# Kernel optimization log

Hardware: AMD Instinct MI355X
Metric: run time of the kernel (lower is better)

## Reference

```python
import jax, jax.numpy as jnp
import numpy as np

N, E, U, EF, STEPS = 5000, 40000, 64, 16, 4


def setup_inputs() -> dict:
    key = jax.random.key(0)
    ks = jax.random.split(key, 7)
    node_features = jax.random.normal(ks[0], (N, U), dtype=jnp.float32)
    edge_features = jax.random.normal(ks[1], (E, EF), dtype=jnp.float32)
    pair_indices = jax.random.randint(ks[2], (E, 2), 0, N, dtype=jnp.int32)
    # EdgeNetwork params: kernel (efc, nfc*nfc), bias (nfc*nfc,)
    edge_kernel = jax.random.normal(ks[3], (EF, U * U), dtype=jnp.float32) * 0.05
    edge_bias = jnp.zeros((U * U,), dtype=jnp.float32)
    # Keras GRUCell (reset_after=True): kernel (in, 3u), recurrent (u, 3u), bias (2, 3u)
    gru_kernel = jax.random.normal(ks[4], (U, 3 * U), dtype=jnp.float32) * 0.05
    gru_recurrent_kernel = jax.random.normal(ks[5], (U, 3 * U), dtype=jnp.float32) * 0.05
    gru_bias = jnp.zeros((2, 3 * U), dtype=jnp.float32)
    return {
        "node_features": node_features,
        "edge_features": edge_features,
        "pair_indices": pair_indices,
        "edge_kernel": edge_kernel,
        "edge_bias": edge_bias,
        "gru_kernel": gru_kernel,
        "gru_recurrent_kernel": gru_recurrent_kernel,
        "gru_bias": gru_bias,
    }


def _gru_cell(x, h, kernel, rkernel, bias):
    # Keras GRUCell math with reset_after=True
    u = h.shape[-1]
    mx = x @ kernel + bias[0]          # [N, 3u]
    mh = h @ rkernel + bias[1]         # [N, 3u]
    xz, xr, xh = mx[:, :u], mx[:, u:2 * u], mx[:, 2 * u:]
    iz, ir, ih = mh[:, :u], mh[:, u:2 * u], mh[:, 2 * u:]
    z = jax.nn.sigmoid(xz + iz)
    r = jax.nn.sigmoid(xr + ir)
    hh = jnp.tanh(xh + r * ih)
    return z * h + (1.0 - z) * hh


def reference(node_features, edge_features, pair_indices, edge_kernel, edge_bias,
              gru_kernel, gru_recurrent_kernel, gru_bias):
    n = node_features.shape[0]
    u = node_features.shape[1]  # units (pad_length = 0 since nfc == units)
    src = pair_indices[:, 0]
    nbr = pair_indices[:, 1]
    # Edge matrices are loop-invariant: [E, u, u]
    edge_mats = (edge_features @ edge_kernel + edge_bias).reshape(-1, u, u)
    h = node_features
    for _ in range(STEPS):
        nb = h[nbr]                                    # gather [E, u]
        msg = jnp.einsum('eij,ej->ei', edge_mats, nb)  # per-edge matvec
        agg = jax.ops.segment_sum(msg, src, num_segments=n)  # scatter-sum [N, u]
        h = _gru_cell(agg, h, gru_kernel, gru_recurrent_kernel, gru_bias)
    return h
```

## Files before the change

kernel.cpp:

```cpp
#include <hip/hip_runtime.h>
#include <math.h>

#define NN 5000
#define NE 40000
#define UU 64
#define FE 16
#define FEP 17
#define KD (FEP*UU)
#define LDK (KD+8)
#define NSTEPS 4
#define NT 8
#define NB (NN/NT)
#define EMAX 256
#define CH 8

typedef _Float16 half8 __attribute__((ext_vector_type(8)));
typedef float f32x4 __attribute__((ext_vector_type(4)));

__device__ __forceinline__ float sigm(float x){ return 1.f/(1.f + __expf(-x)); }
__device__ __forceinline__ int rfl(int x){ return __builtin_amdgcn_readfirstlane(x); }

#define WBN (UU*KD)
#define GTN (192*64)
__global__ void build_k(const float* __restrict__ ek, const float* __restrict__ eb,
                        const float* __restrict__ gk, const float* __restrict__ rk,
                        _Float16* __restrict__ wb, _Float16* __restrict__ gkt,
                        _Float16* __restrict__ rkt, int* __restrict__ offs){
  int tid = blockIdx.x*blockDim.x + threadIdx.x;
  if (tid <= NN) offs[tid] = 0;
  if (tid < WBN){
    int i = tid / KD, k = tid - i*KD;
    int f = k >> 6, j = k & 63;
    float v = (f < FE) ? ek[f*4096 + i*64 + j] : eb[i*64 + j];
    wb[tid] = (_Float16)v;
  } else if (tid < WBN + GTN){
    int r = tid - WBN; int n = r >> 6, k = r & 63;
    gkt[r] = (_Float16)gk[k*192 + n];
  } else if (tid < WBN + 2*GTN){
    int r = tid - WBN - GTN; int n = r >> 6, k = r & 63;
    rkt[r] = (_Float16)rk[k*192 + n];
  }
}

__global__ void hist_k(const int* __restrict__ pair, int* __restrict__ hist){
  int e = blockIdx.x*blockDim.x + threadIdx.x;
  if (e < NE) atomicAdd(&hist[pair[2*e]], 1);
}

__global__ void scan_k(int* __restrict__ offs, int* __restrict__ cursor){
  __shared__ int s[1024];
  const int PER = 5;
  int t = threadIdx.x;
  int base = t*PER;
  int loc[PER]; int sum = 0;
  #pragma unroll
  for (int q=0;q<PER;++q){ int idx = base+q; int v = (idx<NN)?offs[idx]:0; loc[q]=v; sum+=v; }
  s[t] = sum; __syncthreads();
  for (int off=1; off<1024; off<<=1){
    int v = (t>=off) ? s[t-off] : 0;
    __syncthreads();
    s[t] += v;
    __syncthreads();
  }
  int run = s[t] - sum;
  #pragma unroll
  for (int q=0;q<PER;++q){ int idx = base+q;
    if (idx<NN){ offs[idx]=run; cursor[idx]=run; run+=loc[q]; } }
  if (t==1023) offs[NN] = run;
}

__global__ void scatter_k(const int* __restrict__ pair, int* __restrict__ cursor,
                          int* __restrict__ eid){
  int e = blockIdx.x*blockDim.x + threadIdx.x;
  if (e < NE){ int pos = atomicAdd(&cursor[pair[2*e]], 1); eid[pos] = e; }
}

__global__ void sortsub_k(const int* __restrict__ offs, int* __restrict__ eid){
  int v = blockIdx.x*blockDim.x + threadIdx.x;
  if (v >= NN) return;
  int b = offs[v], e = offs[v+1];
  for (int i=b+1; i<e; ++i){
    int key = eid[i]; int j = i-1;
    while (j>=b && eid[j]>key){ eid[j+1]=eid[j]; --j; }
    eid[j+1] = key;
  }
}

__global__ __launch_bounds__(512) void step_k(const float* __restrict__ h_in,
        float* __restrict__ h_out,
        const int* __restrict__ pair, const float* __restrict__ ef,
        const int* __restrict__ offs, const int* __restrict__ eid,
        const _Float16* __restrict__ wb, const _Float16* __restrict__ gkt,
        const _Float16* __restrict__ rkt, const float* __restrict__ gb){
  __shared__ _Float16 Gs[NT*LDK];
  __shared__ int      enbr[EMAX];
  __shared__ int      eedg[EMAX];
  __shared__ _Float16 aggT[NT*72];
  __shared__ _Float16 hT[NT*72];

  int tid = threadIdx.x;
  int w = tid >> 6, lane = tid & 63;
  int r16 = lane & 15, kh = lane >> 4;
  int vb = blockIdx.x * NT;

  int ebase = offs[vb];
  int ecnt  = offs[vb + NT] - ebase;

  for (int i=tid; i<ecnt; i+=512){
    int e = eid[ebase + i];
    enbr[i] = pair[2*e + 1];
    eedg[i] = e;
  }
  hT[w*72 + lane] = (_Float16)h_in[(size_t)(vb + w)*64 + lane];
  __syncthreads();

  {
    int myb = offs[vb + w]     - ebase;
    int mye = offs[vb + w + 1] - ebase;
    float g[FEP];
    #pragma unroll
    for (int f=0;f<FEP;++f) g[f] = 0.f;
    for (int c0=myb; c0<mye; c0+=CH){
      float hj[CH];
      #pragma unroll
      for (int q=0;q<CH;++q){ int i=c0+q;
        if (i<mye){ int nb = rfl(enbr[i]); hj[q] = h_in[(size_t)nb*64 + lane]; }
        else hj[q] = 0.f; }
      #pragma unroll
      for (int q=0;q<CH;++q){ int i=c0+q;
        if (i<mye){
          int e = rfl(eedg[i]);
          const float4* er = (const float4*)(ef + (size_t)e*FE);
          float4 e0 = er[0], e1 = er[1], e2 = er[2], e3 = er[3];
          g[ 0]=fmaf(e0.x,hj[q],g[ 0]); g[ 1]=fmaf(e0.y,hj[q],g[ 1]);
          g[ 2]=fmaf(e0.z,hj[q],g[ 2]); g[ 3]=fmaf(e0.w,hj[q],g[ 3]);
          g[ 4]=fmaf(e1.x,hj[q],g[ 4]); g[ 5]=fmaf(e1.y,hj[q],g[ 5]);
          g[ 6]=fmaf(e1.z,hj[q],g[ 6]); g[ 7]=fmaf(e1.w,hj[q],g[ 7]);
          g[ 8]=fmaf(e2.x,hj[q],g[ 8]); g[ 9]=fmaf(e2.y,hj[q],g[ 9]);
          g[10]=fmaf(e2.z,hj[q],g[10]); g[11]=fmaf(e2.w,hj[q],g[11]);
          g[12]=fmaf(e3.x,hj[q],g[12]); g[13]=fmaf(e3.y,hj[q],g[13]);
          g[14]=fmaf(e3.z,hj[q],g[14]); g[15]=fmaf(e3.w,hj[q],g[15]);
          g[16] += hj[q];
        } }
    }
    #pragma unroll
    for (int f=0;f<FEP;++f) Gs[w*LDK + f*64 + lane] = (_Float16)g[f];
  }
  __syncthreads();

  if (w < 4){
    f32x4 acc = {0.f,0.f,0.f,0.f};
    const _Float16* ap = Gs + (r16 & 7)*LDK + kh*8;
    const _Float16* bp = wb + (size_t)(w*16 + r16)*KD + kh*8;
    #pragma unroll 2
    for (int k0=0; k0<KD; k0+=32){
      half8 a = *(const half8*)(ap + k0);
      half8 b = *(const half8*)(bp + k0);
      acc = __builtin_amdgcn_mfma_f32_16x16x32_f16(a, b, acc, 0, 0, 0);
    }
    if (kh < 2){
      #pragma unroll
      for (int r=0;r<4;++r) aggT[(kh*4+r)*72 + w*16 + r16] = (_Float16)acc[r];
    }
  }
  __syncthreads();

  if (w < 4){
    int uw = w*16 + r16;
    const _Float16* az = aggT + (r16 & 7)*72 + kh*8;
    const _Float16* ah = hT   + (r16 & 7)*72 + kh*8;
    f32x4 mxz={0.f,0.f,0.f,0.f}, mxr=mxz, mxh=mxz, mhz=mxz, mhr=mxz, mhh=mxz;
    #pragma unroll
    for (int ks=0; ks<2; ++ks){
      half8 aa = *(const half8*)(az + ks*32);
      half8 hh = *(const half8*)(ah + ks*32);
      half8 bz = *(const half8*)(gkt + (size_t)(      uw)*64 + ks*32 + kh*8);
      half8 br = *(const half8*)(gkt + (size_t)( 64 + uw)*64 + ks*32 + kh*8);
      half8 bh = *(const half8*)(gkt + (size_t)(128 + uw)*64 + ks*32 + kh*8);
      half8 cz = *(const half8*)(rkt + (size_t)(      uw)*64 + ks*32 + kh*8);
      half8 cr = *(const half8*)(rkt + (size_t)( 64 + uw)*64 + ks*32 + kh*8);
      half8 ch = *(const half8*)(rkt + (size_t)(128 + uw)*64 + ks*32 + kh*8);
      mxz = __builtin_amdgcn_mfma_f32_16x16x32_f16(aa, bz, mxz, 0,0,0);
      mxr = __builtin_amdgcn_mfma_f32_16x16x32_f16(aa, br, mxr, 0,0,0);
      mxh = __builtin_amdgcn_mfma_f32_16x16x32_f16(aa, bh, mxh, 0,0,0);
      mhz = __builtin_amdgcn_mfma_f32_16x16x32_f16(hh, cz, mhz, 0,0,0);
      mhr = __builtin_amdgcn_mfma_f32_16x16x32_f16(hh, cr, mhr, 0,0,0);
      mhh = __builtin_amdgcn_mfma_f32_16x16x32_f16(hh, ch, mhh, 0,0,0);
    }
    if (kh < 2){
      float b0z = gb[uw],      b0r = gb[64+uw],  b0h = gb[128+uw];
      float b1z = gb[192+uw],  b1r = gb[256+uw], b1h = gb[320+uw];
      #pragma unroll
      for (int r=0;r<4;++r){
        int row = vb + kh*4 + r;
        float z  = sigm(mxz[r] + b0z + mhz[r] + b1z);
        float rr = sigm(mxr[r] + b0r + mhr[r] + b1r);
        float hc = tanhf(mxh[r] + b0h + rr*(mhh[r] + b1h));
        float hold = h_in[(size_t)row*64 + uw];
        h_out[(size_t)row*64 + uw] = z*hold + (1.f - z)*hc;
      }
    }
  }
}

extern "C" void kernel_launch(void* const* d_in, const int* in_sizes, int n_in,
                              void* d_out, int out_size, void* d_ws, size_t ws_size,
                              hipStream_t stream){
  const float* nodef = (const float*)d_in[0];
  const float* edgef = (const float*)d_in[1];
  const int*   pair  = (const int*)  d_in[2];
  const float* ek    = (const float*)d_in[3];
  const float* ebias = (const float*)d_in[4];
  const float* gk    = (const float*)d_in[5];
  const float* rk    = (const float*)d_in[6];
  const float* gb    = (const float*)d_in[7];

  char* ws = (char*)d_ws;
  size_t o = 0;
  auto carve = [&](size_t bytes)->char*{
    char* p = ws + o; o = (o + bytes + 255) & ~255ULL; return p; };
  int*      offs   = (int*)     carve((NN+1)*sizeof(int));
  int*      cursor = (int*)     carve(NN*sizeof(int));
  int*      eid    = (int*)     carve(NE*sizeof(int));
  _Float16* wb     = (_Float16*)carve((size_t)WBN*sizeof(_Float16));
  _Float16* gkt    = (_Float16*)carve((size_t)GTN*sizeof(_Float16));
  _Float16* rkt    = (_Float16*)carve((size_t)GTN*sizeof(_Float16));
  float*    hA     = (float*)   carve((size_t)NN*UU*sizeof(float));
  float*    hB     = (float*)   carve((size_t)NN*UU*sizeof(float));

  build_k  <<<(WBN+2*GTN+255)/256, 256, 0, stream>>>(ek, ebias, gk, rk, wb, gkt, rkt, offs);
  hist_k   <<<(NE+255)/256, 256, 0, stream>>>(pair, offs);
  scan_k   <<<1, 1024, 0, stream>>>(offs, cursor);
  scatter_k<<<(NE+255)/256, 256, 0, stream>>>(pair, cursor, eid);
  sortsub_k<<<(NN+255)/256, 256, 0, stream>>>(offs, eid);

  const float* hin = nodef;
  for (int s=0; s<NSTEPS; ++s){
    float* hout = (s == NSTEPS-1) ? (float*)d_out : ((s & 1) ? hB : hA);
    step_k<<<NB, 512, 0, stream>>>(hin, hout, pair, edgef, offs, eid,
                                   wb, gkt, rkt, gb);
    hin = hout;
  }
}
```

Before: 143.3 us.

## Fuse preprocessing and all GRU steps into one cooperative persistent kernel

Replaces the nine separate launches (weight conversion, histogram, scan, scatter, per-node sort and four step kernels) with one cooperative kernel of 256 persistent blocks. Phases are separated by grid-wide syncs, and the per-node edge sort moves into the first step. The node tile grows from 8 to 16 so the 16-row MFMA tiles are fully used instead of half-padded. The aim is to remove per-launch overhead and wasted MFMA rows. The cost is grid syncs, a serial scan on a single block, and uneven work because 313 tiles are spread over 256 blocks.

```diff
diff --git a/kernel.cpp b/kernel.cpp
--- a/kernel.cpp
+++ b/kernel.cpp
@@ -1,5 +1,8 @@
 #include <hip/hip_runtime.h>
+#include <hip/hip_cooperative_groups.h>
 #include <math.h>
+
+namespace cg = cooperative_groups;
 
 #define NN 5000
 #define NE 40000
@@ -9,10 +12,13 @@
 #define KD (FEP*UU)
 #define LDK (KD+8)
 #define NSTEPS 4
-#define NT 8
-#define NB (NN/NT)
-#define EMAX 256
+#define NT 16
+#define NTILES 313
+#define GRID 256
+#define EMAX 1024
 #define CH 8
+#define WBN (UU*KD)
+#define GTN (192*64)
 
 typedef _Float16 half8 __attribute__((ext_vector_type(8)));
 typedef float f32x4 __attribute__((ext_vector_type(4)));
@@ -20,186 +26,196 @@
 __device__ __forceinline__ float sigm(float x){ return 1.f/(1.f + __expf(-x)); }
 __device__ __forceinline__ int rfl(int x){ return __builtin_amdgcn_readfirstlane(x); }
 
-#define WBN (UU*KD)
-#define GTN (192*64)
-__global__ void build_k(const float* __restrict__ ek, const float* __restrict__ eb,
-                        const float* __restrict__ gk, const float* __restrict__ rk,
-                        _Float16* __restrict__ wb, _Float16* __restrict__ gkt,
-                        _Float16* __restrict__ rkt, int* __restrict__ offs){
-  int tid = blockIdx.x*blockDim.x + threadIdx.x;
-  if (tid <= NN) offs[tid] = 0;
-  if (tid < WBN){
-    int i = tid / KD, k = tid - i*KD;
-    int f = k >> 6, j = k & 63;
-    float v = (f < FE) ? ek[f*4096 + i*64 + j] : eb[i*64 + j];
-    wb[tid] = (_Float16)v;
-  } else if (tid < WBN + GTN){
-    int r = tid - WBN; int n = r >> 6, k = r & 63;
-    gkt[r] = (_Float16)gk[k*192 + n];
-  } else if (tid < WBN + 2*GTN){
-    int r = tid - WBN - GTN; int n = r >> 6, k = r & 63;
-    rkt[r] = (_Float16)rk[k*192 + n];
-  }
-}
-
-__global__ void hist_k(const int* __restrict__ pair, int* __restrict__ hist){
-  int e = blockIdx.x*blockDim.x + threadIdx.x;
-  if (e < NE) atomicAdd(&hist[pair[2*e]], 1);
-}
-
-__global__ void scan_k(int* __restrict__ offs, int* __restrict__ cursor){
-  __shared__ int s[1024];
-  const int PER = 5;
-  int t = threadIdx.x;
-  int base = t*PER;
-  int loc[PER]; int sum = 0;
-  #pragma unroll
-  for (int q=0;q<PER;++q){ int idx = base+q; int v = (idx<NN)?offs[idx]:0; loc[q]=v; sum+=v; }
-  s[t] = sum; __syncthreads();
-  for (int off=1; off<1024; off<<=1){
-    int v = (t>=off) ? s[t-off] : 0;
-    __syncthreads();
-    s[t] += v;
-    __syncthreads();
-  }
-  int run = s[t] - sum;
-  #pragma unroll
-  for (int q=0;q<PER;++q){ int idx = base+q;
-    if (idx<NN){ offs[idx]=run; cursor[idx]=run; run+=loc[q]; } }
-  if (t==1023) offs[NN] = run;
-}
-
-__global__ void scatter_k(const int* __restrict__ pair, int* __restrict__ cursor,
-                          int* __restrict__ eid){
-  int e = blockIdx.x*blockDim.x + threadIdx.x;
-  if (e < NE){ int pos = atomicAdd(&cursor[pair[2*e]], 1); eid[pos] = e; }
-}
-
-__global__ void sortsub_k(const int* __restrict__ offs, int* __restrict__ eid){
-  int v = blockIdx.x*blockDim.x + threadIdx.x;
-  if (v >= NN) return;
-  int b = offs[v], e = offs[v+1];
-  for (int i=b+1; i<e; ++i){
-    int key = eid[i]; int j = i-1;
-    while (j>=b && eid[j]>key){ eid[j+1]=eid[j]; --j; }
-    eid[j+1] = key;
-  }
-}
-
-__global__ __launch_bounds__(512) void step_k(const float* __restrict__ h_in,
-        float* __restrict__ h_out,
-        const int* __restrict__ pair, const float* __restrict__ ef,
-        const int* __restrict__ offs, const int* __restrict__ eid,
-        const _Float16* __restrict__ wb, const _Float16* __restrict__ gkt,
-        const _Float16* __restrict__ rkt, const float* __restrict__ gb){
+__global__ __launch_bounds__(512, 2) void mega_k(
+    const float* __restrict__ nodef, const float* __restrict__ edgef,
+    const int* __restrict__ pair,   const float* __restrict__ ek,
+    const float* __restrict__ eb,   const float* __restrict__ gk,
+    const float* __restrict__ rk,   const float* __restrict__ gb,
+    int* __restrict__ offs, int* __restrict__ cursor, int* __restrict__ eid,
+    _Float16* __restrict__ wb, _Float16* __restrict__ gkt, _Float16* __restrict__ rkt,
+    float* __restrict__ hA, float* __restrict__ hB, float* __restrict__ dout){
+
   __shared__ _Float16 Gs[NT*LDK];
   __shared__ int      enbr[EMAX];
   __shared__ int      eedg[EMAX];
   __shared__ _Float16 aggT[NT*72];
   __shared__ _Float16 hT[NT*72];
 
+  cg::grid_group grid = cg::this_grid();
   int tid = threadIdx.x;
+  int gt  = blockIdx.x*512 + tid;
   int w = tid >> 6, lane = tid & 63;
   int r16 = lane & 15, kh = lane >> 4;
-  int vb = blockIdx.x * NT;
-
-  int ebase = offs[vb];
-  int ecnt  = offs[vb + NT] - ebase;
-
-  for (int i=tid; i<ecnt; i+=512){
-    int e = eid[ebase + i];
-    enbr[i] = pair[2*e + 1];
-    eedg[i] = e;
+
+  if (gt <= NN) offs[gt] = 0;
+  if (gt < WBN){
+    int i = gt / KD, k = gt - i*KD;
+    int f = k >> 6, j = k & 63;
+    float v = (f < FE) ? ek[f*4096 + i*64 + j] : eb[i*64 + j];
+    wb[gt] = (_Float16)v;
+  } else if (gt < WBN + GTN){
+    int r = gt - WBN; int n = r >> 6, k = r & 63;
+    gkt[r] = (_Float16)gk[k*192 + n];
+  } else if (gt < WBN + 2*GTN){
+    int r = gt - WBN - GTN; int n = r >> 6, k = r & 63;
+    rkt[r] = (_Float16)rk[k*192 + n];
   }
-  hT[w*72 + lane] = (_Float16)h_in[(size_t)(vb + w)*64 + lane];
-  __syncthreads();
-
-  {
-    int myb = offs[vb + w]     - ebase;
-    int mye = offs[vb + w + 1] - ebase;
-    float g[FEP];
+  grid.sync();
+
+  if (gt < NE) atomicAdd(&offs[pair[2*gt]], 1);
+  grid.sync();
+
+  if (blockIdx.x == 0){
+    int* sArr = (int*)Gs;
+    const int PER = 10;
+    int base = tid*PER;
+    int loc[PER]; int sum = 0;
     #pragma unroll
-    for (int f=0;f<FEP;++f) g[f] = 0.f;
-    for (int c0=myb; c0<mye; c0+=CH){
-      float hj[CH];
+    for (int q=0;q<PER;++q){ int idx=base+q; int v=(idx<NN)?offs[idx]:0; loc[q]=v; sum+=v; }
+    sArr[tid] = sum; __syncthreads();
+    for (int off=1; off<512; off<<=1){
+      int v = (tid>=off) ? sArr[tid-off] : 0;
+      __syncthreads();
+      sArr[tid] += v;
+      __syncthreads();
+    }
+    int run = sArr[tid] - sum;
+    #pragma unroll
+    for (int q=0;q<PER;++q){ int idx=base+q;
+      if (idx<NN){ offs[idx]=run; cursor[idx]=run; run+=loc[q]; } }
+    if (tid==511) offs[NN] = NE;
+  }
+  grid.sync();
+
+  if (gt < NE){ int pos = atomicAdd(&cursor[pair[2*gt]], 1); eid[pos] = gt; }
+  grid.sync();
+
+  for (int s=0; s<NSTEPS; ++s){
+    const float* h_in  = (s==0) ? nodef : ((s&1) ? hA : hB);
+    float*       h_out = (s==NSTEPS-1) ? dout : ((s&1) ? hB : hA);
+
+    for (int t = blockIdx.x; t < NTILES; t += GRID){
+      int vb = t * NT;
+      int vtop = (vb + NT < NN) ? vb + NT : NN;
+
+      if (s == 0){
+        if (tid < NT && vb + tid < NN){
+          int b = offs[vb+tid], e = offs[vb+tid+1];
+          for (int i=b+1; i<e; ++i){
+            int key = eid[i]; int j = i-1;
+            while (j>=b && eid[j]>key){ eid[j+1]=eid[j]; --j; }
+            eid[j+1] = key;
+          }
+        }
+        __syncthreads();
+      }
+
+      int ebase = offs[vb];
+      int ecnt  = offs[vtop] - ebase;
+
+      for (int i=tid; i<ecnt; i+=512){
+        int e = eid[ebase + i];
+        enbr[i] = pair[2*e + 1];
+        eedg[i] = e;
+      }
+      for (int i=tid; i<NT*64; i+=512){
+        int lv = i >> 6, j = i & 63; int v = vb + lv;
+        hT[lv*72 + j] = (_Float16)((v < NN) ? h_in[(size_t)v*64 + j] : 0.f);
+      }
+      __syncthreads();
+
       #pragma unroll
-      for (int q=0;q<CH;++q){ int i=c0+q;
-        if (i<mye){ int nb = rfl(enbr[i]); hj[q] = h_in[(size_t)nb*64 + lane]; }
-        else hj[q] = 0.f; }
-      #pragma unroll
-      for (int q=0;q<CH;++q){ int i=c0+q;
-        if (i<mye){
-          int e = rfl(eedg[i]);
-          const float4* er = (const float4*)(ef + (size_t)e*FE);
-          float4 e0 = er[0], e1 = er[1], e2 = er[2], e3 = er[3];
-          g[ 0]=fmaf(e0.x,hj[q],g[ 0]); g[ 1]=fmaf(e0.y,hj[q],g[ 1]);
-          g[ 2]=fmaf(e0.z,hj[q],g[ 2]); g[ 3]=fmaf(e0.w,hj[q],g[ 3]);
-          g[ 4]=fmaf(e1.x,hj[q],g[ 4]); g[ 5]=fmaf(e1.y,hj[q],g[ 5]);
-          g[ 6]=fmaf(e1.z,hj[q],g[ 6]); g[ 7]=fmaf(e1.w,hj[q],g[ 7]);
-          g[ 8]=fmaf(e2.x,hj[q],g[ 8]); g[ 9]=fmaf(e2.y,hj[q],g[ 9]);
-          g[10]=fmaf(e2.z,hj[q],g[10]); g[11]=fmaf(e2.w,hj[q],g[11]);
-          g[12]=fmaf(e3.x,hj[q],g[12]); g[13]=fmaf(e3.y,hj[q],g[13]);
-          g[14]=fmaf(e3.z,hj[q],g[14]); g[15]=fmaf(e3.w,hj[q],g[15]);
-          g[16] += hj[q];
-        } }
+      for (int nn=0; nn<2; ++nn){
+        int node = vb + w*2 + nn;
+        if (node < NN){
+          int myb = offs[node]   - ebase;
+          int mye = offs[node+1] - ebase;
+          float g[FEP];
+          #pragma unroll
+          for (int f=0;f<FEP;++f) g[f] = 0.f;
+          for (int c0=myb; c0<mye; c0+=CH){
+            float hj[CH];
+            #pragma unroll
+            for (int q=0;q<CH;++q){ int i=c0+q;
+              if (i<mye){ int nb = rfl(enbr[i]); hj[q] = h_in[(size_t)nb*64 + lane]; }
+              else hj[q] = 0.f; }
+            #pragma unroll
+            for (int q=0;q<CH;++q){ int i=c0+q;
+              if (i<mye){
+                int e = rfl(eedg[i]);
+                const float4* er = (const float4*)(edgef + (size_t)e*FE);
+                float4 e0 = er[0], e1 = er[1], e2 = er[2], e3 = er[3];
+                g[ 0]=fmaf(e0.x,hj[q],g[ 0]); g[ 1]=fmaf(e0.y,hj[q],g[ 1]);
+                g[ 2]=fmaf(e0.z,hj[q],g[ 2]); g[ 3]=fmaf(e0.w,hj[q],g[ 3]);
+                g[ 4]=fmaf(e1.x,hj[q],g[ 4]); g[ 5]=fmaf(e1.y,hj[q],g[ 5]);
+                g[ 6]=fmaf(e1.z,hj[q],g[ 6]); g[ 7]=fmaf(e1.w,hj[q],g[ 7]);
+                g[ 8]=fmaf(e2.x,hj[q],g[ 8]); g[ 9]=fmaf(e2.y,hj[q],g[ 9]);
+                g[10]=fmaf(e2.z,hj[q],g[10]); g[11]=fmaf(e2.w,hj[q],g[11]);
+                g[12]=fmaf(e3.x,hj[q],g[12]); g[13]=fmaf(e3.y,hj[q],g[13]);
+                g[14]=fmaf(e3.z,hj[q],g[14]); g[15]=fmaf(e3.w,hj[q],g[15]);
+                g[16] += hj[q];
+              } }
+          }
+          #pragma unroll
+          for (int f=0;f<FEP;++f) Gs[(w*2+nn)*LDK + f*64 + lane] = (_Float16)g[f];
+        }
+      }
+      __syncthreads();
+
+      if (w < 4){
+        f32x4 acc = {0.f,0.f,0.f,0.f};
+        const _Float16* ap = Gs + r16*LDK + kh*8;
+        const _Float16* bp = wb + (size_t)(w*16 + r16)*KD + kh*8;
+        #pragma unroll 2
+        for (int k0=0; k0<KD; k0+=32){
+          half8 a = *(const half8*)(ap + k0);
+          half8 b = *(const half8*)(bp + k0);
+          acc = __builtin_amdgcn_mfma_f32_16x16x32_f16(a, b, acc, 0, 0, 0);
+        }
+        #pragma unroll
+        for (int r=0;r<4;++r) aggT[(kh*4+r)*72 + w*16 + r16] = (_Float16)acc[r];
+      }
+      __syncthreads();
+
+      if (w < 4){
+        int uw = w*16 + r16;
+        const _Float16* az = aggT + r16*72 + kh*8;
+        const _Float16* ah = hT   + r16*72 + kh*8;
+        f32x4 mxz={0.f,0.f,0.f,0.f}, mxr=mxz, mxh=mxz, mhz=mxz, mhr=mxz, mhh=mxz;
+        #pragma unroll
+        for (int ks=0; ks<2; ++ks){
+          half8 aa = *(const half8*)(az + ks*32);
+          half8 hh = *(const half8*)(ah + ks*32);
+          half8 bz = *(const half8*)(gkt + (size_t)(      uw)*64 + ks*32 + kh*8);
+          half8 br = *(const half8*)(gkt + (size_t)( 64 + uw)*64 + ks*32 + kh*8);
+          half8 bh = *(const half8*)(gkt + (size_t)(128 + uw)*64 + ks*32 + kh*8);
+          half8 cz = *(const half8*)(rkt + (size_t)(      uw)*64 + ks*32 + kh*8);
+          half8 cr = *(const half8*)(rkt + (size_t)( 64 + uw)*64 + ks*32 + kh*8);
+          half8 ch = *(const half8*)(rkt + (size_t)(128 + uw)*64 + ks*32 + kh*8);
+          mxz = __builtin_amdgcn_mfma_f32_16x16x32_f16(aa, bz, mxz, 0,0,0);
+          mxr = __builtin_amdgcn_mfma_f32_16x16x32_f16(aa, br, mxr, 0,0,0);
+          mxh = __builtin_amdgcn_mfma_f32_16x16x32_f16(aa, bh, mxh, 0,0,0);
+          mhz = __builtin_amdgcn_mfma_f32_16x16x32_f16(hh, cz, mhz, 0,0,0);
+          mhr = __builtin_amdgcn_mfma_f32_16x16x32_f16(hh, cr, mhr, 0,0,0);
+          mhh = __builtin_amdgcn_mfma_f32_16x16x32_f16(hh, ch, mhh, 0,0,0);
+        }
+        float b0z = gb[uw],      b0r = gb[64+uw],  b0h = gb[128+uw];
+        float b1z = gb[192+uw],  b1r = gb[256+uw], b1h = gb[320+uw];
+        #pragma unroll
+        for (int r=0;r<4;++r){
+          int row = vb + kh*4 + r;
+          if (row < NN){
+            float z  = sigm(mxz[r] + b0z + mhz[r] + b1z);
+            float rr = sigm(mxr[r] + b0r + mhr[r] + b1r);
+            float hc = tanhf(mxh[r] + b0h + rr*(mhh[r] + b1h));
+            float hold = h_in[(size_t)row*64 + uw];
+            h_out[(size_t)row*64 + uw] = z*hold + (1.f - z)*hc;
+          }
+        }
+      }
+      __syncthreads();
     }
-    #pragma unroll
-    for (int f=0;f<FEP;++f) Gs[w*LDK + f*64 + lane] = (_Float16)g[f];
-  }
-  __syncthreads();
-
-  if (w < 4){
-    f32x4 acc = {0.f,0.f,0.f,0.f};
-    const _Float16* ap = Gs + (r16 & 7)*LDK + kh*8;
-    const _Float16* bp = wb + (size_t)(w*16 + r16)*KD + kh*8;
-    #pragma unroll 2
-    for (int k0=0; k0<KD; k0+=32){
-      half8 a = *(const half8*)(ap + k0);
-      half8 b = *(const half8*)(bp + k0);
-      acc = __builtin_amdgcn_mfma_f32_16x16x32_f16(a, b, acc, 0, 0, 0);
-    }
-    if (kh < 2){
-      #pragma unroll
-      for (int r=0;r<4;++r) aggT[(kh*4+r)*72 + w*16 + r16] = (_Float16)acc[r];
-    }
-  }
-  __syncthreads();
-
-  if (w < 4){
-    int uw = w*16 + r16;
-    const _Float16* az = aggT + (r16 & 7)*72 + kh*8;
-    const _Float16* ah = hT   + (r16 & 7)*72 + kh*8;
-    f32x4 mxz={0.f,0.f,0.f,0.f}, mxr=mxz, mxh=mxz, mhz=mxz, mhr=mxz, mhh=mxz;
-    #pragma unroll
-    for (int ks=0; ks<2; ++ks){
-      half8 aa = *(const half8*)(az + ks*32);
-      half8 hh = *(const half8*)(ah + ks*32);
-      half8 bz = *(const half8*)(gkt + (size_t)(      uw)*64 + ks*32 + kh*8);
-      half8 br = *(const half8*)(gkt + (size_t)( 64 + uw)*64 + ks*32 + kh*8);
-      half8 bh = *(const half8*)(gkt + (size_t)(128 + uw)*64 + ks*32 + kh*8);
-      half8 cz = *(const half8*)(rkt + (size_t)(      uw)*64 + ks*32 + kh*8);
-      half8 cr = *(const half8*)(rkt + (size_t)( 64 + uw)*64 + ks*32 + kh*8);
-      half8 ch = *(const half8*)(rkt + (size_t)(128 + uw)*64 + ks*32 + kh*8);
-      mxz = __builtin_amdgcn_mfma_f32_16x16x32_f16(aa, bz, mxz, 0,0,0);
-      mxr = __builtin_amdgcn_mfma_f32_16x16x32_f16(aa, br, mxr, 0,0,0);
-      mxh = __builtin_amdgcn_mfma_f32_16x16x32_f16(aa, bh, mxh, 0,0,0);
-      mhz = __builtin_amdgcn_mfma_f32_16x16x32_f16(hh, cz, mhz, 0,0,0);
-      mhr = __builtin_amdgcn_mfma_f32_16x16x32_f16(hh, cr, mhr, 0,0,0);
-      mhh = __builtin_amdgcn_mfma_f32_16x16x32_f16(hh, ch, mhh, 0,0,0);
-    }
-    if (kh < 2){
-      float b0z = gb[uw],      b0r = gb[64+uw],  b0h = gb[128+uw];
-      float b1z = gb[192+uw],  b1r = gb[256+uw], b1h = gb[320+uw];
-      #pragma unroll
-      for (int r=0;r<4;++r){
-        int row = vb + kh*4 + r;
-        float z  = sigm(mxz[r] + b0z + mhz[r] + b1z);
-        float rr = sigm(mxr[r] + b0r + mhr[r] + b1r);
-        float hc = tanhf(mxh[r] + b0h + rr*(mhh[r] + b1h));
-        float hold = h_in[(size_t)row*64 + uw];
-        h_out[(size_t)row*64 + uw] = z*hold + (1.f - z)*hc;
-      }
-    }
+    if (s < NSTEPS-1) grid.sync();
   }
 }
 
@@ -214,6 +230,7 @@
   const float* gk    = (const float*)d_in[5];
   const float* rk    = (const float*)d_in[6];
   const float* gb    = (const float*)d_in[7];
+  float*       dout  = (float*)d_out;
 
   char* ws = (char*)d_ws;
   size_t o = 0;
@@ -228,17 +245,10 @@
   float*    hA     = (float*)   carve((size_t)NN*UU*sizeof(float));
   float*    hB     = (float*)   carve((size_t)NN*UU*sizeof(float));
 
-  build_k  <<<(WBN+2*GTN+255)/256, 256, 0, stream>>>(ek, ebias, gk, rk, wb, gkt, rkt, offs);
-  hist_k   <<<(NE+255)/256, 256, 0, stream>>>(pair, offs);
-  scan_k   <<<1, 1024, 0, stream>>>(offs, cursor);
-  scatter_k<<<(NE+255)/256, 256, 0, stream>>>(pair, cursor, eid);
-  sortsub_k<<<(NN+255)/256, 256, 0, stream>>>(offs, eid);
-
-  const float* hin = nodef;
-  for (int s=0; s<NSTEPS; ++s){
-    float* hout = (s == NSTEPS-1) ? (float*)d_out : ((s & 1) ? hB : hA);
-    step_k<<<NB, 512, 0, stream>>>(hin, hout, pair, edgef, offs, eid,
-                                   wb, gkt, rkt, gb);
-    hin = hout;
-  }
+  void* args[] = { (void*)&nodef, (void*)&edgef, (void*)&pair, (void*)&ek,
+                   (void*)&ebias, (void*)&gk, (void*)&rk, (void*)&gb,
+                   (void*)&offs, (void*)&cursor, (void*)&eid,
+                   (void*)&wb, (void*)&gkt, (void*)&rkt,
+                   (void*)&hA, (void*)&hB, (void*)&dout };
+  hipLaunchCooperativeKernel((void*)mega_k, dim3(GRID), dim3(512), args, 0, stream);
 }
```

New measurement: 350.6 us. 145% more time.
